# Performance work log

Measured on AMD Instinct MI355X. Metric: run time of the kernel, lower is better.

The kernel has to match this reference:

```python
import jax, jax.numpy as jnp
import numpy as np


def setup_inputs() -> dict:
    key = jax.random.key(0)
    kx, kq, kk, kv = jax.random.split(key, 4)
    B, S, D = 4, 2048, 1024
    return {
        "x": jax.random.normal(kx, (B, S, D), dtype=jnp.float32),
        "Wq": jax.random.normal(kq, (D, D), dtype=jnp.float32),
        "Wk": jax.random.normal(kk, (D, D), dtype=jnp.float32),
        "Wv": jax.random.normal(kv, (D, D), dtype=jnp.float32),
    }


def reference(x, Wq, Wk, Wv):
    # x: [B, S, D]; single-head self-attention, output concat([x, attn], axis=-1)
    D = x.shape[-1]
    Q = jnp.einsum("bsd,de->bse", x, Wq)
    K = jnp.einsum("bsd,de->bse", x, Wk)
    V = jnp.einsum("bsd,de->bse", x, Wv)
    scale = 1.0 / jnp.sqrt(jnp.float32(D))
    scores = jax.nn.softmax(jnp.einsum("bqd,bkd->bqk", Q, K) * scale, axis=-1)  # [B,S,S]
    attn = jnp.einsum("bqk,bkd->bqd", scores, V)
    return jnp.concatenate([x, attn], axis=2)  # [B, S, 2D]
```

## Files before the change

kernel.cpp:

```cpp
#include <hip/hip_runtime.h>
#include <stdint.h>


typedef _Float16 h8 __attribute__((ext_vector_type(8)));
typedef _Float16 h4 __attribute__((ext_vector_type(4)));
typedef float    f4 __attribute__((ext_vector_type(4)));

#define BAR() __builtin_amdgcn_s_barrier()
#define LGKM0_FENCE()                                      \
  asm volatile("s_waitcnt lgkmcnt(0)" ::: "memory");       \
  __builtin_amdgcn_sched_barrier(0)

template <int N>
__device__ __forceinline__ void vmw() {
  if constexpr (N == 0) asm volatile("s_waitcnt vmcnt(0)" ::: "memory");
  else if constexpr (N == 1) asm volatile("s_waitcnt vmcnt(1)" ::: "memory");
  else if constexpr (N == 2) asm volatile("s_waitcnt vmcnt(2)" ::: "memory");
  else if constexpr (N == 3) asm volatile("s_waitcnt vmcnt(3)" ::: "memory");
  else if constexpr (N == 4) asm volatile("s_waitcnt vmcnt(4)" ::: "memory");
  else if constexpr (N == 5) asm volatile("s_waitcnt vmcnt(5)" ::: "memory");
  else if constexpr (N == 6) asm volatile("s_waitcnt vmcnt(6)" ::: "memory");
}

__device__ __forceinline__ void gl_lds16(const _Float16* g, _Float16* l) {
  __builtin_amdgcn_global_load_lds(
      (const __attribute__((address_space(1))) unsigned int*)g,
      (__attribute__((address_space(3))) unsigned int*)l, 16, 0, 0);
}

__global__ __launch_bounds__(256) void prep_x_split_copy(
    const float* __restrict__ x, _Float16* __restrict__ xh,
    _Float16* __restrict__ xl, float* __restrict__ out) {
  size_t i = (size_t)blockIdx.x * 256 + threadIdx.x;
  f4 v = ((const f4*)x)[i];
  h4 hi, lo;
#pragma unroll
  for (int j = 0; j < 4; ++j) {
    _Float16 h = (_Float16)v[j];
    hi[j] = h;
    lo[j] = (_Float16)(v[j] - (float)h);
  }
  ((h4*)xh)[i] = hi;
  ((h4*)xl)[i] = lo;
  size_t r = i >> 8, c = i & 255;
  ((f4*)out)[r * 512 + c] = v;
}

__global__ __launch_bounds__(256) void prep_w_split(const float* __restrict__ W,
                                                    _Float16* __restrict__ WTh,
                                                    _Float16* __restrict__ WTl) {
  int i = blockIdx.x * 256 + threadIdx.x;
  int d = i >> 10, e = i & 1023;
  float v = W[i];
  _Float16 h = (_Float16)v;
  WTh[e * 1024 + d] = h;
  if (WTl) WTl[e * 1024 + d] = (_Float16)(v - (float)h);
}

enum { EM_F32 = 0, EM_QK = 1, EM_VT = 2 };

struct G8 {
  const _Float16* Areg[3]; long zA; int lda;
  const _Float16* Breg[4][3]; long zB; int ldb;
  int NT[4];
  int emode[4];
  float* Cf; long zC; int ldc; float scale;
  _Float16* Ch[4]; _Float16* Cl[4];
  _Float16* Vt;
};

template <int BM, int BN>
__global__ __launch_bounds__(512, 2) void gemmdp(G8 p) {
  constexpr int MFR = BM / 32;
  constexpr int MPH = MFR / 2;
  constexpr int NFR = BN / 64;
  constexpr int NPH = NFR / 2;
  constexpr int LA = BM / 128;
  constexpr int LB = BN / 128;
  __shared__ alignas(16) _Float16 ldsA[2][BM][64];
  __shared__ alignas(16) _Float16 ldsB[2][BN][64];

  const int t0 = threadIdx.x;
  const int lane = t0 & 63;
  const int w = t0 >> 6;
  const int wm = w >> 2, wn = w & 3;
  const int l15 = lane & 15, l4 = lane >> 4;

  const int nbx = gridDim.x, nby = gridDim.y;
  const int nwg = nbx * nby * gridDim.z;
  const int bid = blockIdx.x + nbx * (blockIdx.y + nby * blockIdx.z);
  const int nb = (bid & 7) * (nwg >> 3) + (bid >> 3);
  const int bx = nb % nbx, by = (nb / nbx) % nby, z = nb / (nbx * nby);

  const long Mb = (long)by * BM;
  const long Nb = (long)bx * BN;
  const int nt = p.NT[z];
  const long zAo = p.zA * z;
  const long zBo = p.zB * z;
  const int lda = p.lda, ldb = p.ldb;

  const int rr_lo = t0 >> 3;
  const int slot = t0 & 7;
  const int rr0_lo = (t0 & ~63) >> 3;

  f4 acc[MFR][NFR] = {};

  auto stageU = [&](int u, int sb, int kt) {
    const int k0 = kt << 6;
    const int r = k0 >> 10;
    const int cn = k0 & 1023;
    if (u == 0 || u == 3) {
      const _Float16* Ab = p.Areg[r] + zAo + cn;
      const int qm = (u == 3);
      constexpr int QS = BM / 4;
#pragma unroll
      for (int i = 0; i < LA; ++i) {
        int rr = i * 64 + rr_lo;
        int rr0 = i * 64 + rr0_lo;
        int row  = (rr  / QS) * (BM / 2) + qm * QS + (rr  % QS);
        int row0 = (rr0 / QS) * (BM / 2) + qm * QS + (rr0 % QS);
        int scol = (slot ^ (row & 7)) << 3;
        gl_lds16(Ab + (Mb + row) * (long)lda + scol, &ldsA[sb][row0][0]);
      }
    } else {
      const _Float16* Bb = p.Breg[z][r] + zBo + cn;
      const int hh = (u == 2);
      constexpr int QS = BN / 4;
#pragma unroll
      for (int i = 0; i < LB; ++i) {
        int rr = i * 64 + rr_lo;
        int rr0 = i * 64 + rr0_lo;
        int row  = (rr  / QS) * (BN / 2) + hh * QS + (rr  % QS);
        int row0 = (rr0 / QS) * (BN / 2) + hh * QS + (rr0 % QS);
        int scol = (slot ^ (row & 7)) << 3;
        gl_lds16(Bb + (Nb + row) * (long)ldb + scol, &ldsB[sb][row0][0]);
      }
    }
  };

  h8 af[MPH][2];
  h8 bfh[2][NPH][2];

  auto dsA = [&](int qm, int buf) {
#pragma unroll
    for (int m = 0; m < MPH; ++m) {
      int row = wm * (BM / 2) + (qm * MPH + m) * 16 + l15;
#pragma unroll
      for (int ks = 0; ks < 2; ++ks)
        af[m][ks] = *(const h8*)&ldsA[buf][row][(((ks * 4 + l4) ^ (row & 7)) << 3)];
    }
  };
  auto dsB = [&](int hh, int buf) {
#pragma unroll
    for (int n = 0; n < NPH; ++n) {
      int row = wn * (16 * NFR) + (hh * NPH + n) * 16 + l15;
#pragma unroll
      for (int ks = 0; ks < 2; ++ks)
        bfh[hh][n][ks] = *(const h8*)&ldsB[buf][row][(((ks * 4 + l4) ^ (row & 7)) << 3)];
    }
  };
  auto mfmaQ = [&](int qm, int hh) {
    __builtin_amdgcn_s_setprio(1);
#pragma unroll
    for (int ks = 0; ks < 2; ++ks)
#pragma unroll
      for (int m = 0; m < MPH; ++m)
#pragma unroll
        for (int n = 0; n < NPH; ++n)
          acc[qm * MPH + m][hh * NPH + n] = __builtin_amdgcn_mfma_f32_16x16x32_f16(
              af[m][ks], bfh[hh][n][ks], acc[qm * MPH + m][hh * NPH + n], 0, 0, 0);
    __builtin_amdgcn_s_setprio(0);
  };

  constexpr int PRO = 2 * LA + LB;
  constexpr int W0  = 2 * LA + LB;
  constexpr int W1  = LA + 2 * LB;
  constexpr int W3  = 2 * LA + LB;
  constexpr int W3b = LA + LB;
  constexpr int W0c = LA;

  stageU(0, 0, 0); stageU(1, 0, 0); stageU(2, 0, 0); stageU(3, 0, 0);
  stageU(0, 1, 1);
  vmw<PRO>();
  BAR();

  int kt = 0;
  for (; kt + 2 < nt; ++kt) {
    const int buf = kt & 1;
    dsA(0, buf); dsB(0, buf);
    stageU(1, buf ^ 1, kt + 1);
    BAR(); LGKM0_FENCE();
    mfmaQ(0, 0);
    vmw<W0>(); BAR();
    dsB(1, buf);
    stageU(2, buf ^ 1, kt + 1);
    BAR(); LGKM0_FENCE();
    mfmaQ(0, 1);
    vmw<W1>(); BAR();
    dsA(1, buf);
    stageU(3, buf ^ 1, kt + 1);
    BAR(); LGKM0_FENCE();
    mfmaQ(1, 1);
    BAR();
    stageU(0, buf, kt + 2);
    mfmaQ(1, 0);
    vmw<W3>(); BAR();
  }
  {
    const int buf = kt & 1;
    dsA(0, buf); dsB(0, buf);
    stageU(1, buf ^ 1, kt + 1);
    BAR(); LGKM0_FENCE();
    mfmaQ(0, 0);
    vmw<W0>(); BAR();
    dsB(1, buf);
    stageU(2, buf ^ 1, kt + 1);
    BAR(); LGKM0_FENCE();
    mfmaQ(0, 1);
    vmw<W1>(); BAR();
    dsA(1, buf);
    stageU(3, buf ^ 1, kt + 1);
    BAR(); LGKM0_FENCE();
    mfmaQ(1, 1);
    BAR();
    mfmaQ(1, 0);
    vmw<W3b>(); BAR();
    ++kt;
  }
  {
    const int buf = kt & 1;
    dsA(0, buf); dsB(0, buf);
    BAR(); LGKM0_FENCE();
    mfmaQ(0, 0);
    vmw<W0c>(); BAR();
    dsB(1, buf);
    BAR(); LGKM0_FENCE();
    mfmaQ(0, 1);
    vmw<0>(); BAR();
    dsA(1, buf);
    BAR(); LGKM0_FENCE();
    mfmaQ(1, 1);
    mfmaQ(1, 0);
  }

  const int em = p.emode[z];
  const long gr0 = wm * (BM / 2) + l4 * 4;
  const long gc0 = wn * (16 * NFR) + l15;
  if (em == EM_F32) {
    float* C = p.Cf + p.zC * z;
#pragma unroll
    for (int i = 0; i < MFR; ++i)
#pragma unroll
      for (int j = 0; j < NFR; ++j) {
        long gr = Mb + gr0 + i * 16;
        long gc = Nb + gc0 + j * 16;
#pragma unroll
        for (int r = 0; r < 4; ++r)
          C[(gr + r) * (long)p.ldc + gc] = acc[i][j][r] * p.scale;
      }
  } else if (em == EM_QK) {
    _Float16* Ch = p.Ch[z];
    _Float16* Cl = p.Cl[z];
#pragma unroll
    for (int i = 0; i < MFR; ++i)
#pragma unroll
      for (int j = 0; j < NFR; ++j) {
        long gr = Mb + gr0 + i * 16;
        long gc = Nb + gc0 + j * 16;
#pragma unroll
        for (int r = 0; r < 4; ++r) {
          float c = acc[i][j][r];
          _Float16 h = (_Float16)c;
          Ch[(gr + r) * 1024 + gc] = h;
          Cl[(gr + r) * 1024 + gc] = (_Float16)(c - (float)h);
        }
      }
  } else {
    _Float16* Vt = p.Vt;
#pragma unroll
    for (int i = 0; i < MFR; ++i)
#pragma unroll
      for (int j = 0; j < NFR; ++j) {
        long gr = Mb + gr0 + i * 16;
        long gc = Nb + gc0 + j * 16;
        long b = gr >> 11, s = gr & 2047;
        h4 hv;
#pragma unroll
        for (int r = 0; r < 4; ++r) hv[r] = (_Float16)acc[i][j][r];
        *(h4*)&Vt[b * (long)(1024 * 2048) + gc * 2048 + s] = hv;
      }
  }
}

__global__ __launch_bounds__(256) void softmax_rows(float* __restrict__ Sb) {
  const int t = threadIdx.x;
  float* row = Sb + (size_t)blockIdx.x * 2048;
  f4 v0 = ((const f4*)row)[t];
  f4 v1 = ((const f4*)row)[t + 256];
  float mx = -3.0e38f;
#pragma unroll
  for (int j = 0; j < 4; ++j) { mx = fmaxf(mx, v0[j]); mx = fmaxf(mx, v1[j]); }
#pragma unroll
  for (int o = 32; o > 0; o >>= 1) mx = fmaxf(mx, __shfl_xor(mx, o));
  __shared__ float red[4], red2[4];
  const int wave = t >> 6, lane = t & 63;
  if (lane == 0) red[wave] = mx;
  __syncthreads();
  mx = fmaxf(fmaxf(red[0], red[1]), fmaxf(red[2], red[3]));
  float pv[8];
  float sum = 0.f;
#pragma unroll
  for (int j = 0; j < 4; ++j) { pv[j] = __expf(v0[j] - mx); pv[4 + j] = __expf(v1[j] - mx); }
#pragma unroll
  for (int j = 0; j < 8; ++j) sum += pv[j];
#pragma unroll
  for (int o = 32; o > 0; o >>= 1) sum += __shfl_xor(sum, o);
  if (lane == 0) red2[wave] = sum;
  __syncthreads();
  sum = red2[0] + red2[1] + red2[2] + red2[3];
  float inv = 1.0f / sum;
  h4 o0, o1;
#pragma unroll
  for (int j = 0; j < 4; ++j) { o0[j] = (_Float16)(pv[j] * inv); o1[j] = (_Float16)(pv[4 + j] * inv); }
  _Float16* prow = (_Float16*)row;
  ((h4*)prow)[t] = o0;
  ((h4*)prow)[t + 256] = o1;
}

__global__ __launch_bounds__(256) void copy_x_half(const float* __restrict__ x,
                                                   float* __restrict__ out) {
  size_t i = (size_t)blockIdx.x * 256 + threadIdx.x;
  size_t r = i >> 8, c = i & 255;
  ((f4*)out)[r * 512 + c] = ((const f4*)x)[i];
}

__global__ void ws_sentinel(float* out, float v) { out[0] = v; }

extern "C" void kernel_launch(void* const* d_in, const int* in_sizes, int n_in,
                              void* d_out, int out_size, void* d_ws, size_t ws_size,
                              hipStream_t stream) {
  const float* x  = (const float*)d_in[0];
  const float* Wq = (const float*)d_in[1];
  const float* Wk = (const float*)d_in[2];
  const float* Wv = (const float*)d_in[3];
  float* out = (float*)d_out;

  const size_t MB = 1ull << 20;
  char* w = (char*)d_ws;
  _Float16* Qh = (_Float16*)(w + 0 * MB);
  _Float16* Ql = (_Float16*)(w + 16 * MB);
  _Float16* Kh = (_Float16*)(w + 32 * MB);
  _Float16* Kl = (_Float16*)(w + 48 * MB);
  _Float16* VT = (_Float16*)(w + 64 * MB);
  float*    S  = (float*)   (w + 80 * MB);
  _Float16* xh = (_Float16*)(w + 80 * MB);
  _Float16* xl = (_Float16*)(w + 96 * MB);
  _Float16* WqhT = (_Float16*)(w + 112 * MB);
  _Float16* WqlT = (_Float16*)(w + 114 * MB);
  _Float16* WkhT = (_Float16*)(w + 116 * MB);
  _Float16* WklT = (_Float16*)(w + 118 * MB);
  _Float16* WvhT = (_Float16*)(w + 120 * MB);

  if (ws_size < 144 * MB) {
    copy_x_half<<<8192, 256, 0, stream>>>(x, out);
    ws_sentinel<<<1, 1, 0, stream>>>(out, (float)ws_size);
    return;
  }

  prep_x_split_copy<<<8192, 256, 0, stream>>>(x, xh, xl, out);
  prep_w_split<<<4096, 256, 0, stream>>>(Wq, WqhT, WqlT);
  prep_w_split<<<4096, 256, 0, stream>>>(Wk, WkhT, WklT);
  prep_w_split<<<4096, 256, 0, stream>>>(Wv, WvhT, (_Float16*)nullptr);

  G8 pp = {};
  pp.Areg[0] = xh; pp.Areg[1] = xl; pp.Areg[2] = xh; pp.zA = 0; pp.lda = 1024;
  pp.Breg[0][0] = WqhT; pp.Breg[0][1] = WqhT; pp.Breg[0][2] = WqlT;
  pp.Breg[1][0] = WkhT; pp.Breg[1][1] = WkhT; pp.Breg[1][2] = WklT;
  pp.zB = 0; pp.ldb = 1024;
  pp.NT[0] = 48; pp.NT[1] = 48;
  pp.emode[0] = EM_QK; pp.emode[1] = EM_QK;
  pp.Ch[0] = Qh; pp.Cl[0] = Ql; pp.Ch[1] = Kh; pp.Cl[1] = Kl;
  gemmdp<256, 256><<<dim3(4, 32, 2), 512, 0, stream>>>(pp);

  G8 pv = {};
  pv.Areg[0] = xh; pv.Areg[1] = xh; pv.Areg[2] = xh; pv.zA = 0; pv.lda = 1024;
  pv.Breg[0][0] = WvhT; pv.Breg[0][1] = WvhT; pv.Breg[0][2] = WvhT;
  pv.zB = 0; pv.ldb = 1024;
  pv.NT[0] = 16; pv.emode[0] = EM_VT;
  pv.Vt = VT;
  gemmdp<128, 256><<<dim3(4, 64, 1), 512, 0, stream>>>(pv);

  G8 ps = {};
  ps.Areg[0] = Qh; ps.Areg[1] = Ql; ps.Areg[2] = Qh;
  ps.zA = 2048L * 1024; ps.lda = 1024;
  for (int zz = 0; zz < 4; ++zz) {
    ps.Breg[zz][0] = Kh; ps.Breg[zz][1] = Kh; ps.Breg[zz][2] = Kl;
    ps.NT[zz] = 48; ps.emode[zz] = EM_F32;
  }
  ps.zB = 2048L * 1024; ps.ldb = 1024;
  ps.Cf = S; ps.zC = 2048L * 2048; ps.ldc = 2048; ps.scale = 0.03125f;
  gemmdp<256, 256><<<dim3(8, 8, 4), 512, 0, stream>>>(ps);

  softmax_rows<<<8192, 256, 0, stream>>>(S);

  G8 po = {};
  const _Float16* P = (const _Float16*)S;
  po.Areg[0] = P; po.Areg[1] = P + 1024; po.Areg[2] = P;
  po.zA = 2048L * 4096; po.lda = 4096;
  for (int zz = 0; zz < 4; ++zz) {
    po.Breg[zz][0] = VT; po.Breg[zz][1] = VT + 1024; po.Breg[zz][2] = VT;
    po.NT[zz] = 32; po.emode[zz] = EM_F32;
  }
  po.zB = 1024L * 2048; po.ldb = 2048;
  po.Cf = out + 1024; po.zC = 2048L * 2048; po.ldc = 2048; po.scale = 1.f;
  gemmdp<256, 128><<<dim3(8, 8, 4), 512, 0, stream>>>(po);
}
```

Baseline: 338.0 us.

## Fold Wq·Wkᵀ into one matrix, compute x·N then scores against x directly

```diff
diff --git a/kernel.cpp b/kernel.cpp
--- a/kernel.cpp
+++ b/kernel.cpp
@@ -13,13 +13,19 @@
 
 template <int N>
 __device__ __forceinline__ void vmw() {
-  if constexpr (N == 0) asm volatile("s_waitcnt vmcnt(0)" ::: "memory");
-  else if constexpr (N == 1) asm volatile("s_waitcnt vmcnt(1)" ::: "memory");
-  else if constexpr (N == 2) asm volatile("s_waitcnt vmcnt(2)" ::: "memory");
-  else if constexpr (N == 3) asm volatile("s_waitcnt vmcnt(3)" ::: "memory");
-  else if constexpr (N == 4) asm volatile("s_waitcnt vmcnt(4)" ::: "memory");
-  else if constexpr (N == 5) asm volatile("s_waitcnt vmcnt(5)" ::: "memory");
-  else if constexpr (N == 6) asm volatile("s_waitcnt vmcnt(6)" ::: "memory");
+  if constexpr (N == 0)  asm volatile("s_waitcnt vmcnt(0)" ::: "memory");
+  if constexpr (N == 1)  asm volatile("s_waitcnt vmcnt(1)" ::: "memory");
+  if constexpr (N == 2)  asm volatile("s_waitcnt vmcnt(2)" ::: "memory");
+  if constexpr (N == 3)  asm volatile("s_waitcnt vmcnt(3)" ::: "memory");
+  if constexpr (N == 4)  asm volatile("s_waitcnt vmcnt(4)" ::: "memory");
+  if constexpr (N == 5)  asm volatile("s_waitcnt vmcnt(5)" ::: "memory");
+  if constexpr (N == 6)  asm volatile("s_waitcnt vmcnt(6)" ::: "memory");
+  if constexpr (N == 7)  asm volatile("s_waitcnt vmcnt(7)" ::: "memory");
+  if constexpr (N == 8)  asm volatile("s_waitcnt vmcnt(8)" ::: "memory");
+  if constexpr (N == 9)  asm volatile("s_waitcnt vmcnt(9)" ::: "memory");
+  if constexpr (N == 10) asm volatile("s_waitcnt vmcnt(10)" ::: "memory");
+  if constexpr (N == 11) asm volatile("s_waitcnt vmcnt(11)" ::: "memory");
+  if constexpr (N == 12) asm volatile("s_waitcnt vmcnt(12)" ::: "memory");
 }
 
 __device__ __forceinline__ void gl_lds16(const _Float16* g, _Float16* l) {
@@ -46,15 +52,27 @@
   ((f4*)out)[r * 512 + c] = v;
 }
 
-__global__ __launch_bounds__(256) void prep_w_split(const float* __restrict__ W,
-                                                    _Float16* __restrict__ WTh,
-                                                    _Float16* __restrict__ WTl) {
+__global__ __launch_bounds__(256) void prep_w_noT(const float* __restrict__ W,
+                                                  _Float16* __restrict__ Wh,
+                                                  _Float16* __restrict__ Wl) {
+  size_t i = (size_t)blockIdx.x * 256 + threadIdx.x;
+  f4 v = ((const f4*)W)[i];
+  h4 hi, lo;
+#pragma unroll
+  for (int j = 0; j < 4; ++j) {
+    _Float16 h = (_Float16)v[j];
+    hi[j] = h;
+    lo[j] = (_Float16)(v[j] - (float)h);
+  }
+  ((h4*)Wh)[i] = hi;
+  ((h4*)Wl)[i] = lo;
+}
+
+__global__ __launch_bounds__(256) void prep_w_T(const float* __restrict__ W,
+                                                _Float16* __restrict__ WTh) {
   int i = blockIdx.x * 256 + threadIdx.x;
   int d = i >> 10, e = i & 1023;
-  float v = W[i];
-  _Float16 h = (_Float16)v;
-  WTh[e * 1024 + d] = h;
-  if (WTl) WTl[e * 1024 + d] = (_Float16)(v - (float)h);
+  WTh[e * 1024 + d] = (_Float16)W[i];
 }
 
 enum { EM_F32 = 0, EM_QK = 1, EM_VT = 2 };
@@ -125,13 +143,13 @@
     } else {
       const _Float16* Bb = p.Breg[z][r] + zBo + cn;
       const int hh = (u == 2);
-      constexpr int QS = BN / 4;
+      constexpr int BQ = BN / 8;
 #pragma unroll
       for (int i = 0; i < LB; ++i) {
         int rr = i * 64 + rr_lo;
         int rr0 = i * 64 + rr0_lo;
-        int row  = (rr  / QS) * (BN / 2) + hh * QS + (rr  % QS);
-        int row0 = (rr0 / QS) * (BN / 2) + hh * QS + (rr0 % QS);
+        int row  = (rr  / BQ) * (BN / 4) + hh * BQ + (rr  % BQ);
+        int row0 = (rr0 / BQ) * (BN / 4) + hh * BQ + (rr0 % BQ);
         int scol = (slot ^ (row & 7)) << 3;
         gl_lds16(Bb + (Nb + row) * (long)ldb + scol, &ldsB[sb][row0][0]);
       }
@@ -172,59 +190,56 @@
     __builtin_amdgcn_s_setprio(0);
   };
 
-  constexpr int PRO = 2 * LA + LB;
-  constexpr int W0  = 2 * LA + LB;
-  constexpr int W1  = LA + 2 * LB;
-  constexpr int W3  = 2 * LA + LB;
-  constexpr int W3b = LA + LB;
-  constexpr int W0c = LA;
+  constexpr int W_P0 = 3 * LA + 2 * LB;
+  constexpr int W_P1 = 3 * LA + 3 * LB;
+  constexpr int W_P3 = 3 * LA + 3 * LB;
+  constexpr int TP0  = 3 * LA + 2 * LB;
+  constexpr int TP1  = 2 * LA + 2 * LB;
+  constexpr int TP3  = LA + LB;
+  constexpr int UP0  = LA;
 
   stageU(0, 0, 0); stageU(1, 0, 0); stageU(2, 0, 0); stageU(3, 0, 0);
-  stageU(0, 1, 1);
-  vmw<PRO>();
+  stageU(0, 1, 1); stageU(1, 1, 1); stageU(2, 1, 1); stageU(3, 1, 1);
+  vmw<W_P3>();
   BAR();
 
   int kt = 0;
   for (; kt + 2 < nt; ++kt) {
     const int buf = kt & 1;
     dsA(0, buf); dsB(0, buf);
-    stageU(1, buf ^ 1, kt + 1);
     BAR(); LGKM0_FENCE();
     mfmaQ(0, 0);
-    vmw<W0>(); BAR();
+    vmw<W_P0>(); BAR();
     dsB(1, buf);
-    stageU(2, buf ^ 1, kt + 1);
+    stageU(0, buf, kt + 2); stageU(1, buf, kt + 2);
     BAR(); LGKM0_FENCE();
     mfmaQ(0, 1);
-    vmw<W1>(); BAR();
+    vmw<W_P1>(); BAR();
     dsA(1, buf);
-    stageU(3, buf ^ 1, kt + 1);
+    stageU(2, buf, kt + 2);
     BAR(); LGKM0_FENCE();
     mfmaQ(1, 1);
     BAR();
-    stageU(0, buf, kt + 2);
+    stageU(3, buf, kt + 2);
     mfmaQ(1, 0);
-    vmw<W3>(); BAR();
+    vmw<W_P3>(); BAR();
   }
   {
     const int buf = kt & 1;
     dsA(0, buf); dsB(0, buf);
-    stageU(1, buf ^ 1, kt + 1);
     BAR(); LGKM0_FENCE();
     mfmaQ(0, 0);
-    vmw<W0>(); BAR();
+    vmw<TP0>(); BAR();
     dsB(1, buf);
-    stageU(2, buf ^ 1, kt + 1);
     BAR(); LGKM0_FENCE();
     mfmaQ(0, 1);
-    vmw<W1>(); BAR();
+    vmw<TP1>(); BAR();
     dsA(1, buf);
-    stageU(3, buf ^ 1, kt + 1);
     BAR(); LGKM0_FENCE();
     mfmaQ(1, 1);
     BAR();
     mfmaQ(1, 0);
-    vmw<W3b>(); BAR();
+    vmw<TP3>(); BAR();
     ++kt;
   }
   {
@@ -232,7 +247,7 @@
     dsA(0, buf); dsB(0, buf);
     BAR(); LGKM0_FENCE();
     mfmaQ(0, 0);
-    vmw<W0c>(); BAR();
+    vmw<UP0>(); BAR();
     dsB(1, buf);
     BAR(); LGKM0_FENCE();
     mfmaQ(0, 1);
@@ -347,19 +362,19 @@
 
   const size_t MB = 1ull << 20;
   char* w = (char*)d_ws;
-  _Float16* Qh = (_Float16*)(w + 0 * MB);
-  _Float16* Ql = (_Float16*)(w + 16 * MB);
-  _Float16* Kh = (_Float16*)(w + 32 * MB);
-  _Float16* Kl = (_Float16*)(w + 48 * MB);
+  _Float16* Th = (_Float16*)(w + 0 * MB);
+  _Float16* Tl = (_Float16*)(w + 16 * MB);
+  _Float16* xh = (_Float16*)(w + 32 * MB);
+  _Float16* xl = (_Float16*)(w + 48 * MB);
   _Float16* VT = (_Float16*)(w + 64 * MB);
   float*    S  = (float*)   (w + 80 * MB);
-  _Float16* xh = (_Float16*)(w + 80 * MB);
-  _Float16* xl = (_Float16*)(w + 96 * MB);
-  _Float16* WqhT = (_Float16*)(w + 112 * MB);
-  _Float16* WqlT = (_Float16*)(w + 114 * MB);
-  _Float16* WkhT = (_Float16*)(w + 116 * MB);
-  _Float16* WklT = (_Float16*)(w + 118 * MB);
-  _Float16* WvhT = (_Float16*)(w + 120 * MB);
+  _Float16* Wqh = (_Float16*)(w + 80 * MB);
+  _Float16* Wql = (_Float16*)(w + 82 * MB);
+  _Float16* Wkh = (_Float16*)(w + 84 * MB);
+  _Float16* Wkl = (_Float16*)(w + 86 * MB);
+  _Float16* WvT = (_Float16*)(w + 88 * MB);
+  _Float16* Nh  = (_Float16*)(w + 90 * MB);
+  _Float16* Nl  = (_Float16*)(w + 92 * MB);
 
   if (ws_size < 144 * MB) {
     copy_x_half<<<8192, 256, 0, stream>>>(x, out);
@@ -368,33 +383,39 @@
   }
 
   prep_x_split_copy<<<8192, 256, 0, stream>>>(x, xh, xl, out);
-  prep_w_split<<<4096, 256, 0, stream>>>(Wq, WqhT, WqlT);
-  prep_w_split<<<4096, 256, 0, stream>>>(Wk, WkhT, WklT);
-  prep_w_split<<<4096, 256, 0, stream>>>(Wv, WvhT, (_Float16*)nullptr);
-
-  G8 pp = {};
-  pp.Areg[0] = xh; pp.Areg[1] = xl; pp.Areg[2] = xh; pp.zA = 0; pp.lda = 1024;
-  pp.Breg[0][0] = WqhT; pp.Breg[0][1] = WqhT; pp.Breg[0][2] = WqlT;
-  pp.Breg[1][0] = WkhT; pp.Breg[1][1] = WkhT; pp.Breg[1][2] = WklT;
-  pp.zB = 0; pp.ldb = 1024;
-  pp.NT[0] = 48; pp.NT[1] = 48;
-  pp.emode[0] = EM_QK; pp.emode[1] = EM_QK;
-  pp.Ch[0] = Qh; pp.Cl[0] = Ql; pp.Ch[1] = Kh; pp.Cl[1] = Kl;
-  gemmdp<256, 256><<<dim3(4, 32, 2), 512, 0, stream>>>(pp);
+  prep_w_noT<<<1024, 256, 0, stream>>>(Wq, Wqh, Wql);
+  prep_w_noT<<<1024, 256, 0, stream>>>(Wk, Wkh, Wkl);
+  prep_w_T<<<4096, 256, 0, stream>>>(Wv, WvT);
+
+  G8 pn = {};
+  pn.Areg[0] = Wkh; pn.Areg[1] = Wkl; pn.Areg[2] = Wkh; pn.zA = 0; pn.lda = 1024;
+  pn.Breg[0][0] = Wqh; pn.Breg[0][1] = Wqh; pn.Breg[0][2] = Wql;
+  pn.zB = 0; pn.ldb = 1024;
+  pn.NT[0] = 48; pn.emode[0] = EM_QK;
+  pn.Ch[0] = Nh; pn.Cl[0] = Nl;
+  gemmdp<128, 128><<<dim3(8, 8, 1), 512, 0, stream>>>(pn);
+
+  G8 pt = {};
+  pt.Areg[0] = xh; pt.Areg[1] = xl; pt.Areg[2] = xh; pt.zA = 0; pt.lda = 1024;
+  pt.Breg[0][0] = Nh; pt.Breg[0][1] = Nh; pt.Breg[0][2] = Nl;
+  pt.zB = 0; pt.ldb = 1024;
+  pt.NT[0] = 48; pt.emode[0] = EM_QK;
+  pt.Ch[0] = Th; pt.Cl[0] = Tl;
+  gemmdp<256, 128><<<dim3(8, 32, 1), 512, 0, stream>>>(pt);
 
   G8 pv = {};
   pv.Areg[0] = xh; pv.Areg[1] = xh; pv.Areg[2] = xh; pv.zA = 0; pv.lda = 1024;
-  pv.Breg[0][0] = WvhT; pv.Breg[0][1] = WvhT; pv.Breg[0][2] = WvhT;
+  pv.Breg[0][0] = WvT; pv.Breg[0][1] = WvT; pv.Breg[0][2] = WvT;
   pv.zB = 0; pv.ldb = 1024;
   pv.NT[0] = 16; pv.emode[0] = EM_VT;
   pv.Vt = VT;
   gemmdp<128, 256><<<dim3(4, 64, 1), 512, 0, stream>>>(pv);
 
   G8 ps = {};
-  ps.Areg[0] = Qh; ps.Areg[1] = Ql; ps.Areg[2] = Qh;
+  ps.Areg[0] = Th; ps.Areg[1] = Tl; ps.Areg[2] = Th;
   ps.zA = 2048L * 1024; ps.lda = 1024;
   for (int zz = 0; zz < 4; ++zz) {
-    ps.Breg[zz][0] = Kh; ps.Breg[zz][1] = Kh; ps.Breg[zz][2] = Kl;
+    ps.Breg[zz][0] = xh; ps.Breg[zz][1] = xh; ps.Breg[zz][2] = xl;
     ps.NT[zz] = 48; ps.emode[zz] = EM_F32;
   }
   ps.zB = 2048L * 1024; ps.ldb = 1024;
```

Result: slower. 357.6 us (+5.8%).
